# Kernel optimization log

Measured on AMD Instinct MI355X. Metric: run time of the kernel, lower is better.

## Reference

```python
import jax, jax.numpy as jnp
import numpy as np

BATCH, T, HID = 4, 2048, 1024
H = P = 1024  # input_dim and ssm_size (expand_ratio=1.0)
EPS = 1e-5
DISCRETIZATION = "IM"  # 'IM' or 'IMEX'


def setup_inputs() -> dict:
    key = jax.random.key(0)
    ks = jax.random.split(key, 10)
    std_b = 1.0 / np.sqrt(H)
    std_c = 1.0 / np.sqrt(P)
    u = lambda k, s, lo, hi: jax.random.uniform(k, s, jnp.float32, lo, hi)
    return {
        "hidden_states": jax.random.normal(ks[0], (BATCH, T, HID), jnp.float32),
        "Wi": jax.random.normal(ks[1], (H, HID), jnp.float32) / np.sqrt(HID),
        "Wg": jax.random.normal(ks[2], (H, HID), jnp.float32) / np.sqrt(HID),
        "Wo": jax.random.normal(ks[3], (HID, H), jnp.float32) / np.sqrt(H),
        "A_diag": u(ks[4], (P,), 0.0, 1.0),
        "B_param": u(ks[5], (P, H, 2), -std_b, std_b),
        "C_param": u(ks[6], (H, P, 2), -std_c, std_c),
        "D": jax.random.normal(ks[7], (H,), jnp.float32),
        "dt": u(ks[8], (P,), 0.0, 1.0),
        "norm_weight": jnp.ones((H,), jnp.float32),
    }


def _linoss(x, B_param, C_param, A_diag, dt_p, D):
    """LinOSS oscillatory SSM recurrence with complex B/C and diagonal A.
    x: (B,T,H) real input. State z,y in C^P (re/im stacked on last axis)."""
    A = jax.nn.relu(A_diag)       # (P,) nonneg frequencies
    dt = jax.nn.sigmoid(dt_p)     # (P,) timesteps in (0,1)
    # Bu_{re,im}[b,t,p] = sum_h x[b,t,h] * B_{re,im}[p,h]
    Bu = jnp.einsum('bth,phc->btpc', x, B_param)  # (B,T,P,2)
    if DISCRETIZATION == "IM":
        S = 1.0 / (1.0 + dt * dt * A)
        m11, m12, m21, m22 = S, -dt * A * S, dt * S, S
        f1, f2 = dt * S, dt * dt * S
    else:  # IMEX
        one = jnp.ones_like(dt)
        m11, m12, m21, m22 = one, -dt * A, dt, 1.0 - dt * dt * A
        f1, f2 = dt, dt * dt
    c = lambda v: v[None, :, None]  # broadcast (P,) -> (B,P,2)

    def step(carry, bu):
        z, y = carry  # each (B,P,2)
        z1 = c(m11) * z + c(m12) * y + c(f1) * bu
        y1 = c(m21) * z + c(m22) * y + c(f2) * bu
        return (z1, y1), y1

    z0 = jnp.zeros((x.shape[0], A.shape[0], 2), x.dtype)
    _, ys = jax.lax.scan(step, (z0, z0), jnp.swapaxes(Bu, 0, 1))
    ys = jnp.swapaxes(ys, 0, 1)  # (B,T,P,2)
    # o = Re(C @ y) + D * x
    o = (jnp.einsum('btp,hp->bth', ys[..., 0], C_param[..., 0])
         - jnp.einsum('btp,hp->bth', ys[..., 1], C_param[..., 1]))
    return o + x * D


def reference(hidden_states, Wi, Wg, Wo, A_diag, B_param, C_param, D, dt, norm_weight):
    x = hidden_states @ Wi.T                        # i_proj
    o = _linoss(x, B_param, C_param, A_diag, dt, D)  # fused_recurrent_linoss
    g = hidden_states @ Wg.T                        # g_proj
    # FusedRMSNormGated: rmsnorm(o) * weight * swish(g)
    o = o * jax.lax.rsqrt(jnp.mean(o * o, axis=-1, keepdims=True) + EPS) * norm_weight
    o = o * (g * jax.nn.sigmoid(g))
    return o @ Wo.T                                  # o_proj
```

## Files before the change

### kernel.cpp

```cpp
#include <hip/hip_runtime.h>
#include <hip/hip_bf16.h>
#include <math.h>

#define BB 4
#define TT 2048
#define HH 1024
#define PP 1024
#define MT 8192
#define C2 2048
#define NC 64
#define LCH 32

typedef __attribute__((ext_vector_type(8))) short  bf16x8;
typedef __attribute__((ext_vector_type(4))) float  f32x4;

__device__ __forceinline__ ushort f2bf(float f) {
    union { float f; unsigned u; } v; v.f = f;
    unsigned r = v.u + 0x7fffu + ((v.u >> 16) & 1u);
    return (ushort)(r >> 16);
}
__device__ __forceinline__ float bf2f(ushort h) {
    union { unsigned u; float f; } v; v.u = ((unsigned)h) << 16;
    return v.f;
}

__device__ __forceinline__ void gload16(const ushort* g, ushort* l) {
    __builtin_amdgcn_global_load_lds((const __attribute__((address_space(1))) void*)g,
                                     (__attribute__((address_space(3))) void*)l,
                                     16, 0, 0);
}
__device__ __forceinline__ void barrier_raw() { __builtin_amdgcn_s_barrier(); }
__device__ __forceinline__ void lgk0() { asm volatile("s_waitcnt lgkmcnt(0)" ::: "memory"); }
__device__ __forceinline__ void lgk8() { asm volatile("s_waitcnt lgkmcnt(8)" ::: "memory"); }
__device__ __forceinline__ void vm4()  { asm volatile("s_waitcnt vmcnt(4)"   ::: "memory"); }
__device__ __forceinline__ void vm6()  { asm volatile("s_waitcnt vmcnt(6)"   ::: "memory"); }
__device__ __forceinline__ void vm0()  { asm volatile("s_waitcnt vmcnt(0)"   ::: "memory"); }

#define HS4   (MT * HH / 4)
#define W4    (HH * HH / 4)
#define PREP_CONV  (HS4 + 3 * W4)
#define PREP_B     (PREP_CONV + PP * HH)
#define PREP_TOT   (PREP_B + HH * PP)

__global__ void prep_all(const float* __restrict__ hs, const float* __restrict__ Wi,
                         const float* __restrict__ Wg, const float* __restrict__ Wo,
                         const float* __restrict__ B_param, const float* __restrict__ C_param,
                         ushort* __restrict__ hsb, ushort* __restrict__ Wigb,
                         ushort* __restrict__ Wob, ushort* __restrict__ Bpkb,
                         ushort* __restrict__ Cpkb) {
    int i = blockIdx.x * 256 + threadIdx.x;
    if (i < PREP_CONV) {
        const float4* s;
        ushort4* d;
        if (i < HS4)              { s = (const float4*)hs + i;  d = (ushort4*)hsb + i; }
        else if (i < HS4 + 2*W4)  { int j = i - HS4;
                                    s = (const float4*)(j < W4 ? Wi : Wg) + (j < W4 ? j : j - W4);
                                    d = (ushort4*)Wigb + j; }
        else                      { int j = i - HS4 - 2*W4;
                                    s = (const float4*)Wo + j; d = (ushort4*)Wob + j; }
        float4 v = *s;
        ushort4 o;
        o.x = f2bf(v.x); o.y = f2bf(v.y); o.z = f2bf(v.z); o.w = f2bf(v.w);
        *d = o;
    } else if (i < PREP_B) {
        int idx = i - PREP_CONV;
        int p = idx >> 10;
        int h = idx & 1023;
        float2 v = ((const float2*)B_param)[idx];
        Bpkb[(size_t)p * HH + h]        = f2bf(v.x);
        Bpkb[(size_t)(p + PP) * HH + h] = f2bf(v.y);
    } else {
        int idx = i - PREP_B;
        int h = idx >> 10;
        int p = idx & 1023;
        float2 v = ((const float2*)C_param)[idx];
        Cpkb[(size_t)h * C2 + p]      = f2bf(v.x);
        Cpkb[(size_t)h * C2 + PP + p] = f2bf(-v.y);
    }
}

template<int BM, int STORE_BF16>
__global__ __launch_bounds__(512, 2) void gemm8p(
    const ushort* __restrict__ A, int lda,
    const ushort* __restrict__ B, int ldb,
    void* __restrict__ Cp, int ldc, int K, int nbx)
{
    constexpr int BN  = 256;
    constexpr int MR  = BM / 32;
    constexpr int MRH = MR / 2;
    constexpr int TA  = BM * 128;
    constexpr int TB  = BN * 128;
    __shared__ __align__(16) char smem[2 * TA + 2 * TB];

    const int bid = blockIdx.x;
    const int cpx = gridDim.x >> 3;
    const int wg  = (bid & 7) * cpx + (bid >> 3);
    const int by  = wg / nbx;
    const int bx  = wg - by * nbx;
    const int bm  = by * BM;
    const int bn  = bx * BN;

    const int tid  = threadIdx.x;
    const int wave = tid >> 6;
    const int lane = tid & 63;
    const int wr   = wave >> 2;
    const int wc   = wave & 3;
    const int lr   = lane & 15;
    const int kg   = lane >> 4;

    const int e  = (wave << 10) + ((lane << 4) ^ (((lane >> 3) & 7) << 4));
    const int r0 = e >> 7;
    const int c0 = (e & 127) >> 1;

    auto stA = [&](int bi, int u, int kt) {
        gload16(A + (size_t)(bm + u * 64 + r0) * lda + kt * 64 + c0,
                (ushort*)(smem + bi * TA + u * 8192 + (wave << 10)));
    };
    auto stB = [&](int bi, int u, int kt) {
        gload16(B + (size_t)(bn + u * 64 + r0) * ldb + kt * 64 + c0,
                (ushort*)(smem + 2 * TA + bi * TB + u * 8192 + (wave << 10)));
    };

    bf16x8 Af[MRH][2], Bf[4][2];
    auto ldsA = [&](int bi, int qm) {
#pragma unroll
        for (int f = 0; f < MRH; ++f)
#pragma unroll
            for (int kk = 0; kk < 2; ++kk) {
                int row = wr * (BM / 2) + qm * (BM / 4) + f * 16 + lr;
                int o = row * 128 + kk * 64 + kg * 16;
                o ^= (row & 7) << 4;
                Af[f][kk] = *(const bf16x8*)(smem + bi * TA + o);
            }
    };
    auto ldsBh = [&](int bi, int h) {
#pragma unroll
        for (int n = 0; n < 2; ++n)
#pragma unroll
            for (int kk = 0; kk < 2; ++kk) {
                int row = wc * 64 + (h * 2 + n) * 16 + lr;
                int o = row * 128 + kk * 64 + kg * 16;
                o ^= (row & 7) << 4;
                Bf[h * 2 + n][kk] = *(const bf16x8*)(smem + 2 * TA + bi * TB + o);
            }
    };

    f32x4 acc[MR][4];
#pragma unroll
    for (int m = 0; m < MR; ++m)
#pragma unroll
        for (int n = 0; n < 4; ++n)
#pragma unroll
            for (int i = 0; i < 4; ++i) acc[m][n][i] = 0.f;

    auto mfma16 = [&](int qm, int qn) {
        __builtin_amdgcn_s_setprio(1);
#pragma unroll
        for (int f = 0; f < MRH; ++f)
#pragma unroll
            for (int n2 = 0; n2 < 2; ++n2)
#pragma unroll
                for (int kk = 0; kk < 2; ++kk)
                    acc[qm * MRH + f][qn * 2 + n2] =
                        __builtin_amdgcn_mfma_f32_16x16x32_bf16(
                            Af[f][kk], Bf[qn * 2 + n2][kk],
                            acc[qm * MRH + f][qn * 2 + n2], 0, 0, 0);
        __builtin_amdgcn_s_setprio(0);
    };

    stA(0, 0, 0); stA(0, 1, 0); stA(0, 2, 0); stA(0, 3, 0);
    stB(0, 0, 0); stB(0, 1, 0); stB(0, 2, 0); stB(0, 3, 0);
    stB(1, 0, 1); stB(1, 1, 1); stB(1, 2, 1); stB(1, 3, 1);
    stA(1, 0, 1); stA(1, 2, 1);
    vm6();
    barrier_raw();

    const int nIter = K >> 7;
    for (int J = 0; J < nIter; ++J) {
        const bool pf  = (J + 1 < nIter);
        const int  kt1 = 2 * J + 1, kt2 = 2 * J + 2, kt3 = 2 * J + 3;
        ldsA(0, 0); ldsBh(0, 0);
        stA(1, 1, kt1); stA(1, 3, kt1);
        lgk8();
        barrier_raw(); lgk0(); mfma16(0, 0); barrier_raw();
        ldsBh(0, 1);
        barrier_raw(); lgk0(); mfma16(0, 1); barrier_raw();
        ldsA(0, 1);
        if (pf) { stB(0, 0, kt2); stB(0, 1, kt2); stB(0, 2, kt2); stB(0, 3, kt2); }
        barrier_raw(); lgk0(); mfma16(1, 0); barrier_raw();
        if (pf) { stA(0, 0, kt2); stA(0, 2, kt2); }
        barrier_raw(); lgk0(); mfma16(1, 1);
        if (pf) vm6(); else vm0();
        barrier_raw();
        ldsA(1, 0); ldsBh(1, 0);
        if (pf) { stA(0, 1, kt2); stA(0, 3, kt2); }
        lgk8();
        barrier_raw(); lgk0(); mfma16(0, 0); barrier_raw();
        ldsBh(1, 1);
        barrier_raw(); lgk0(); mfma16(0, 1); barrier_raw();
        ldsA(1, 1);
        if (pf) { stB(1, 0, kt3); stB(1, 1, kt3); stB(1, 2, kt3); stB(1, 3, kt3); }
        barrier_raw(); lgk0(); mfma16(1, 0); barrier_raw();
        if (pf) { stA(1, 0, kt3); stA(1, 2, kt3); }
        barrier_raw(); lgk0(); mfma16(1, 1);
        if (pf) vm6(); else vm0();
        barrier_raw();
    }

#pragma unroll
    for (int mf = 0; mf < MR; ++mf) {
#pragma unroll
        for (int n = 0; n < 4; ++n) {
            int col = bn + wc * 64 + n * 16 + lr;
#pragma unroll
            for (int i = 0; i < 4; ++i) {
                int row = bm + wr * (BM / 2) + mf * 16 + kg * 4 + i;
                float v = acc[mf][n][i];
                if (STORE_BF16)
                    ((ushort*)Cp)[(size_t)row * ldc + col] = f2bf(v);
                else
                    ((float*)Cp)[(size_t)row * ldc + col]  = v;
            }
        }
    }
}

template<int STORE_BF16>
__global__ __launch_bounds__(512, 2) void gemm4p(
    const ushort* __restrict__ A, int lda,
    const ushort* __restrict__ B, int ldb,
    void* __restrict__ Cp, int ldc, int K, int nbx)
{
    constexpr int BM = 128, BN = 256;
    constexpr int TA = BM * 128;
    constexpr int TB = BN * 128;
    __shared__ __align__(16) char smem[2 * TA + 2 * TB];

    const int bid = blockIdx.x;
    const int cpx = gridDim.x >> 3;
    const int wg  = (bid & 7) * cpx + (bid >> 3);
    const int by  = wg / nbx;
    const int bx  = wg - by * nbx;
    const int bm  = by * BM;
    const int bn  = bx * BN;

    const int tid  = threadIdx.x;
    const int wave = tid >> 6;
    const int lane = tid & 63;
    const int wr   = wave >> 2;
    const int wc   = wave & 3;
    const int lr   = lane & 15;
    const int kg   = lane >> 4;

    const int e  = (wave << 10) + ((lane << 4) ^ (((lane >> 3) & 7) << 4));
    const int r0 = e >> 7;
    const int c0 = (e & 127) >> 1;

    auto stA = [&](int bi, int u, int kt) {
        gload16(A + (size_t)(bm + u * 64 + r0) * lda + kt * 64 + c0,
                (ushort*)(smem + bi * TA + u * 8192 + (wave << 10)));
    };
    auto stB = [&](int bi, int u, int kt) {
        gload16(B + (size_t)(bn + u * 64 + r0) * ldb + kt * 64 + c0,
                (ushort*)(smem + 2 * TA + bi * TB + u * 8192 + (wave << 10)));
    };

    bf16x8 Af[2][2], Bf[4][2];
    auto ldsA = [&](int bi, int qm) {
#pragma unroll
        for (int f = 0; f < 2; ++f)
#pragma unroll
            for (int kk = 0; kk < 2; ++kk) {
                int row = wr * 64 + qm * 32 + f * 16 + lr;
                int o = row * 128 + kk * 64 + kg * 16;
                o ^= (row & 7) << 4;
                Af[f][kk] = *(const bf16x8*)(smem + bi * TA + o);
            }
    };
    auto ldsB = [&](int bi) {
#pragma unroll
        for (int n = 0; n < 4; ++n)
#pragma unroll
            for (int kk = 0; kk < 2; ++kk) {
                int row = wc * 64 + n * 16 + lr;
                int o = row * 128 + kk * 64 + kg * 16;
                o ^= (row & 7) << 4;
                Bf[n][kk] = *(const bf16x8*)(smem + 2 * TA + bi * TB + o);
            }
    };

    f32x4 acc[4][4];
#pragma unroll
    for (int m = 0; m < 4; ++m)
#pragma unroll
        for (int n = 0; n < 4; ++n)
#pragma unroll
            for (int i = 0; i < 4; ++i) acc[m][n][i] = 0.f;

    auto cl = [&](int qm) {
        __builtin_amdgcn_s_setprio(1);
#pragma unroll
        for (int f = 0; f < 2; ++f)
#pragma unroll
            for (int n = 0; n < 4; ++n)
#pragma unroll
                for (int kk = 0; kk < 2; ++kk)
                    acc[qm * 2 + f][n] =
                        __builtin_amdgcn_mfma_f32_16x16x32_bf16(
                            Af[f][kk], Bf[n][kk], acc[qm * 2 + f][n], 0, 0, 0);
        __builtin_amdgcn_s_setprio(0);
    };

    stB(0, 0, 0); stB(0, 1, 0); stB(0, 2, 0); stB(0, 3, 0);
    stA(0, 0, 0); stA(0, 1, 0);
    stB(1, 0, 1); stB(1, 1, 1); stB(1, 2, 1); stB(1, 3, 1);
    vm4();
    barrier_raw();

    const int nIter = K >> 7;
    for (int J = 0; J < nIter; ++J) {
        const bool pf  = (J + 1 < nIter);
        const int  kt1 = 2 * J + 1, kt2 = 2 * J + 2, kt3 = 2 * J + 3;
        ldsA(0, 0); ldsB(0);
        stA(1, 0, kt1); stA(1, 1, kt1);
        lgk8();
        barrier_raw();
        cl(0);
        lgk0();
        barrier_raw();
        ldsA(0, 1);
        if (pf) { stB(0, 0, kt2); stB(0, 1, kt2); stB(0, 2, kt2); stB(0, 3, kt2); }
        barrier_raw();
        cl(1);
        lgk0();
        if (pf) vm4(); else vm0();
        barrier_raw();
        ldsA(1, 0); ldsB(1);
        if (pf) { stA(0, 0, kt2); stA(0, 1, kt2); }
        lgk8();
        barrier_raw();
        cl(0);
        lgk0();
        barrier_raw();
        ldsA(1, 1);
        if (pf) { stB(1, 0, kt3); stB(1, 1, kt3); stB(1, 2, kt3); stB(1, 3, kt3); }
        barrier_raw();
        cl(1);
        lgk0();
        if (pf) vm4();
        barrier_raw();
    }

#pragma unroll
    for (int mf = 0; mf < 4; ++mf) {
#pragma unroll
        for (int n = 0; n < 4; ++n) {
            int col = bn + wc * 64 + n * 16 + lr;
#pragma unroll
            for (int i = 0; i < 4; ++i) {
                int row = bm + wr * 64 + mf * 16 + kg * 4 + i;
                float v = acc[mf][n][i];
                if (STORE_BF16)
                    ((ushort*)Cp)[(size_t)row * ldc + col] = f2bf(v);
                else
                    ((float*)Cp)[(size_t)row * ldc + col]  = v;
            }
        }
    }
}

__device__ __forceinline__ void linoss_coeffs(const float* A_diag, const float* dt_p,
                                              int p, float& m11, float& m12,
                                              float& m21, float& m22,
                                              float& f1, float& f2) {
    float A  = fmaxf(A_diag[p], 0.f);
    float dt = 1.f / (1.f + expf(-dt_p[p]));
    float S  = 1.f / (1.f + dt * dt * A);
    m11 = S;        m12 = -dt * A * S;
    m21 = dt * S;   m22 = S;
    f1  = dt * S;   f2  = dt * dt * S;
}

__global__ void scan_passA(const ushort* __restrict__ Bu,
                           const float* __restrict__ A_diag,
                           const float* __restrict__ dt_p,
                           float2* __restrict__ sEnd) {
    int c = blockIdx.x * 256 + threadIdx.x;
    int b = blockIdx.y;
    int j = blockIdx.z;
    float m11, m12, m21, m22, f1, f2;
    linoss_coeffs(A_diag, dt_p, c & 1023, m11, m12, m21, m22, f1, f2);
    const ushort* bu = Bu + ((size_t)(b * TT + j * LCH)) * C2 + c;
    float z = 0.f, y = 0.f;
#pragma unroll 8
    for (int i = 0; i < LCH; ++i) {
        float u  = bf2f(bu[(size_t)i * C2]);
        float z1 = m11 * z + m12 * y + f1 * u;
        float y1 = m21 * z + m22 * y + f2 * u;
        z = z1; y = y1;
    }
    sEnd[((size_t)j * BB + b) * C2 + c] = make_float2(z, y);
}

__global__ void scan_combine(const float* __restrict__ A_diag,
                             const float* __restrict__ dt_p,
                             const float2* __restrict__ sEnd,
                             float2* __restrict__ sInit) {
    int idx = blockIdx.x * 256 + threadIdx.x;
    int c = idx & (C2 - 1);
    int b = idx >> 11;
    float m11, m12, m21, m22, f1, f2;
    linoss_coeffs(A_diag, dt_p, c & 1023, m11, m12, m21, m22, f1, f2);
    float e11 = m11, e12 = m12, e21 = m21, e22 = m22;
#pragma unroll
    for (int s = 0; s < 5; ++s) {
        float n11 = e11 * e11 + e12 * e21;
        float n12 = e11 * e12 + e12 * e22;
        float n21 = e21 * e11 + e22 * e21;
        float n22 = e21 * e12 + e22 * e22;
        e11 = n11; e12 = n12; e21 = n21; e22 = n22;
    }
    float z = 0.f, y = 0.f;
    for (int j = 0; j < NC; ++j) {
        size_t off = ((size_t)j * BB + b) * C2 + c;
        sInit[off] = make_float2(z, y);
        float2 le = sEnd[off];
        float z1 = e11 * z + e12 * y + le.x;
        float y1 = e21 * z + e22 * y + le.y;
        z = z1; y = y1;
    }
}

__global__ void scan_passB(const ushort* __restrict__ Bu,
                           const float* __restrict__ A_diag,
                           const float* __restrict__ dt_p,
                           const float2* __restrict__ sInit,
                           ushort* __restrict__ YSb) {
    int c = blockIdx.x * 256 + threadIdx.x;
    int b = blockIdx.y;
    int j = blockIdx.z;
    float m11, m12, m21, m22, f1, f2;
    linoss_coeffs(A_diag, dt_p, c & 1023, m11, m12, m21, m22, f1, f2);
    float2 s0 = sInit[((size_t)j * BB + b) * C2 + c];
    float z = s0.x, y = s0.y;
    const ushort* bu = Bu  + ((size_t)(b * TT + j * LCH)) * C2 + c;
    ushort*       ys = YSb + ((size_t)(b * TT + j * LCH)) * C2 + c;
#pragma unroll 8
    for (int i = 0; i < LCH; ++i) {
        float u  = bf2f(bu[(size_t)i * C2]);
        float z1 = m11 * z + m12 * y + f1 * u;
        float y1 = m21 * z + m22 * y + f2 * u;
        z = z1; y = y1;
        ys[(size_t)i * C2] = f2bf(y);
    }
}

__global__ void rmsgate_kernel(const ushort* __restrict__ O,
                               const ushort* __restrict__ XGb,
                               const float* __restrict__ Dv,
                               const float* __restrict__ nw,
                               ushort* __restrict__ V) {
    int m = blockIdx.x;
    int t = threadIdx.x;
    ushort4 o4 = ((const ushort4*)(O + (size_t)m * HH))[t];
    ushort4 x4 = ((const ushort4*)(XGb + (size_t)m * C2))[t];
    float4  d4 = ((const float4*)Dv)[t];
    float of[4];
    of[0] = bf2f(o4.x) + d4.x * bf2f(x4.x);
    of[1] = bf2f(o4.y) + d4.y * bf2f(x4.y);
    of[2] = bf2f(o4.z) + d4.z * bf2f(x4.z);
    of[3] = bf2f(o4.w) + d4.w * bf2f(x4.w);
    float ss = of[0]*of[0] + of[1]*of[1] + of[2]*of[2] + of[3]*of[3];
#pragma unroll
    for (int o = 32; o > 0; o >>= 1) ss += __shfl_down(ss, o);
    __shared__ float wsum[4];
    if ((t & 63) == 0) wsum[t >> 6] = ss;
    __syncthreads();
    float tot = wsum[0] + wsum[1] + wsum[2] + wsum[3];
    float r = rsqrtf(tot * (1.f / (float)HH) + 1e-5f);

    ushort4 g4 = ((const ushort4*)(XGb + (size_t)m * C2 + HH))[t];
    float4  w4 = ((const float4*)nw)[t];
    float g[4] = {bf2f(g4.x), bf2f(g4.y), bf2f(g4.z), bf2f(g4.w)};
    float w[4] = {w4.x, w4.y, w4.z, w4.w};
    ushort4 vout;
    ushort* vo = &vout.x;
#pragma unroll
    for (int i = 0; i < 4; ++i) {
        float sw = g[i] / (1.f + expf(-g[i]));
        vo[i] = f2bf(of[i] * r * w[i] * sw);
    }
    ((ushort4*)(V + (size_t)m * HH))[t] = vout;
}

extern "C" void kernel_launch(void* const* d_in, const int* in_sizes, int n_in,
                              void* d_out, int out_size, void* d_ws, size_t ws_size,
                              hipStream_t stream) {
    const float* hs      = (const float*)d_in[0];
    const float* Wi      = (const float*)d_in[1];
    const float* Wg      = (const float*)d_in[2];
    const float* Wo      = (const float*)d_in[3];
    const float* A_diag  = (const float*)d_in[4];
    const float* B_param = (const float*)d_in[5];
    const float* C_param = (const float*)d_in[6];
    const float* Dv      = (const float*)d_in[7];
    const float* dtp     = (const float*)d_in[8];
    const float* nw      = (const float*)d_in[9];
    float* out = (float*)d_out;

    char* ws = (char*)d_ws;
    ushort* hsb  = (ushort*)ws;                                   ws += (size_t)MT * HH * 2;
    ushort* Wigb = (ushort*)ws;                                   ws += (size_t)C2 * HH * 2;
    ushort* Wob  = (ushort*)ws;                                   ws += (size_t)HH * HH * 2;
    ushort* Bpkb = (ushort*)ws;                                   ws += (size_t)C2 * HH * 2;
    ushort* Cpkb = (ushort*)ws;                                   ws += (size_t)HH * C2 * 2;
    ushort* XGb  = (ushort*)ws;                                   ws += (size_t)MT * C2 * 2;
    ushort* Bu   = (ushort*)ws;                                   ws += (size_t)MT * C2 * 2;
    ushort* YSb  = (ushort*)ws;                                   ws += (size_t)MT * C2 * 2;
    ushort* O    = (ushort*)ws;                                   ws += (size_t)MT * HH * 2;
    ushort* Vb   = (ushort*)ws;                                   ws += (size_t)MT * HH * 2;
    float2* sEnd  = (float2*)ws;                                  ws += (size_t)NC * BB * C2 * 8;
    float2* sInit = (float2*)ws;

    dim3 blk(256);

    prep_all<<<dim3(PREP_TOT / 256), blk, 0, stream>>>(
        hs, Wi, Wg, Wo, B_param, C_param, hsb, Wigb, Wob, Bpkb, Cpkb);

    gemm8p<256, 1><<<dim3(256), dim3(512), 0, stream>>>(
        hsb, HH, Wigb, HH, XGb, C2, HH, 8);

    gemm8p<256, 1><<<dim3(256), dim3(512), 0, stream>>>(
        XGb, C2, Bpkb, HH, Bu, C2, HH, 8);

    scan_passA<<<dim3(C2 / 256, BB, NC), blk, 0, stream>>>(Bu, A_diag, dtp, sEnd);
    scan_combine<<<dim3((BB * C2) / 256), blk, 0, stream>>>(A_diag, dtp, sEnd, sInit);
    scan_passB<<<dim3(C2 / 256, BB, NC), blk, 0, stream>>>(Bu, A_diag, dtp, sInit, YSb);

    gemm4p<1><<<dim3(256), dim3(512), 0, stream>>>(
        YSb, C2, Cpkb, C2, O, HH, C2, 4);

    rmsgate_kernel<<<dim3(MT), blk, 0, stream>>>(O, XGb, Dv, nw, Vb);

    gemm4p<0><<<dim3(256), dim3(512), 0, stream>>>(
        Vb, HH, Wob, HH, out, HH, HH, 4);
}
```

Baseline: 188.1 us.

## Use 128x128 tiles with 4-wave blocks and simpler double buffering for N=1024 GEMMs

New measurement: 187.9 us. Within noise of the previous version (-0.1%).

```diff
diff --git a/kernel.cpp b/kernel.cpp
--- a/kernel.cpp
+++ b/kernel.cpp
@@ -32,7 +32,6 @@
 __device__ __forceinline__ void barrier_raw() { __builtin_amdgcn_s_barrier(); }
 __device__ __forceinline__ void lgk0() { asm volatile("s_waitcnt lgkmcnt(0)" ::: "memory"); }
 __device__ __forceinline__ void lgk8() { asm volatile("s_waitcnt lgkmcnt(8)" ::: "memory"); }
-__device__ __forceinline__ void vm4()  { asm volatile("s_waitcnt vmcnt(4)"   ::: "memory"); }
 __device__ __forceinline__ void vm6()  { asm volatile("s_waitcnt vmcnt(6)"   ::: "memory"); }
 __device__ __forceinline__ void vm0()  { asm volatile("s_waitcnt vmcnt(0)"   ::: "memory"); }
 
@@ -226,12 +225,12 @@
 }
 
 template<int STORE_BF16>
-__global__ __launch_bounds__(512, 2) void gemm4p(
+__global__ __launch_bounds__(256, 2) void gemm2b(
     const ushort* __restrict__ A, int lda,
     const ushort* __restrict__ B, int ldb,
     void* __restrict__ Cp, int ldc, int K, int nbx)
 {
-    constexpr int BM = 128, BN = 256;
+    constexpr int BM = 128, BN = 128;
     constexpr int TA = BM * 128;
     constexpr int TB = BN * 128;
     __shared__ __align__(16) char smem[2 * TA + 2 * TB];
@@ -247,8 +246,8 @@
     const int tid  = threadIdx.x;
     const int wave = tid >> 6;
     const int lane = tid & 63;
-    const int wr   = wave >> 2;
-    const int wc   = wave & 3;
+    const int wr   = wave >> 1;
+    const int wc   = wave & 1;
     const int lr   = lane & 15;
     const int kg   = lane >> 4;
 
@@ -257,12 +256,12 @@
     const int c0 = (e & 127) >> 1;
 
     auto stA = [&](int bi, int u, int kt) {
-        gload16(A + (size_t)(bm + u * 64 + r0) * lda + kt * 64 + c0,
-                (ushort*)(smem + bi * TA + u * 8192 + (wave << 10)));
+        gload16(A + (size_t)(bm + u * 32 + r0) * lda + kt * 64 + c0,
+                (ushort*)(smem + bi * TA + u * 4096 + (wave << 10)));
     };
     auto stB = [&](int bi, int u, int kt) {
-        gload16(B + (size_t)(bn + u * 64 + r0) * ldb + kt * 64 + c0,
-                (ushort*)(smem + 2 * TA + bi * TB + u * 8192 + (wave << 10)));
+        gload16(B + (size_t)(bn + u * 32 + r0) * ldb + kt * 64 + c0,
+                (ushort*)(smem + 2 * TA + bi * TB + u * 4096 + (wave << 10)));
     };
 
     bf16x8 Af[2][2], Bf[4][2];
@@ -311,43 +310,29 @@
         __builtin_amdgcn_s_setprio(0);
     };
 
+    stA(0, 0, 0); stA(0, 1, 0); stA(0, 2, 0); stA(0, 3, 0);
     stB(0, 0, 0); stB(0, 1, 0); stB(0, 2, 0); stB(0, 3, 0);
-    stA(0, 0, 0); stA(0, 1, 0);
-    stB(1, 0, 1); stB(1, 1, 1); stB(1, 2, 1); stB(1, 3, 1);
-    vm4();
+    vm0();
     barrier_raw();
 
-    const int nIter = K >> 7;
-    for (int J = 0; J < nIter; ++J) {
-        const bool pf  = (J + 1 < nIter);
-        const int  kt1 = 2 * J + 1, kt2 = 2 * J + 2, kt3 = 2 * J + 3;
-        ldsA(0, 0); ldsB(0);
-        stA(1, 0, kt1); stA(1, 1, kt1);
-        lgk8();
+    const int nT = K >> 6;
+    for (int t = 0; t < nT; ++t) {
+        const int  bt = t & 1, b1 = bt ^ 1;
+        const bool pf = (t + 1 < nT);
+        ldsA(bt, 0); ldsB(bt);
+        if (pf) { stB(b1, 0, t + 1); stB(b1, 1, t + 1);
+                  stB(b1, 2, t + 1); stB(b1, 3, t + 1); }
         barrier_raw();
         cl(0);
         lgk0();
         barrier_raw();
-        ldsA(0, 1);
-        if (pf) { stB(0, 0, kt2); stB(0, 1, kt2); stB(0, 2, kt2); stB(0, 3, kt2); }
+        ldsA(bt, 1);
+        if (pf) { stA(b1, 0, t + 1); stA(b1, 1, t + 1);
+                  stA(b1, 2, t + 1); stA(b1, 3, t + 1); }
         barrier_raw();
         cl(1);
         lgk0();
-        if (pf) vm4(); else vm0();
-        barrier_raw();
-        ldsA(1, 0); ldsB(1);
-        if (pf) { stA(0, 0, kt2); stA(0, 1, kt2); }
-        lgk8();
-        barrier_raw();
-        cl(0);
-        lgk0();
-        barrier_raw();
-        ldsA(1, 1);
-        if (pf) { stB(1, 0, kt3); stB(1, 1, kt3); stB(1, 2, kt3); stB(1, 3, kt3); }
-        barrier_raw();
-        cl(1);
-        lgk0();
-        if (pf) vm4();
+        if (pf) vm0();
         barrier_raw();
     }
 
@@ -537,11 +522,11 @@
     scan_combine<<<dim3((BB * C2) / 256), blk, 0, stream>>>(A_diag, dtp, sEnd, sInit);
     scan_passB<<<dim3(C2 / 256, BB, NC), blk, 0, stream>>>(Bu, A_diag, dtp, sInit, YSb);
 
-    gemm4p<1><<<dim3(256), dim3(512), 0, stream>>>(
-        YSb, C2, Cpkb, C2, O, HH, C2, 4);
+    gemm2b<1><<<dim3(512), dim3(256), 0, stream>>>(
+        YSb, C2, Cpkb, C2, O, HH, C2, 8);
 
     rmsgate_kernel<<<dim3(MT), blk, 0, stream>>>(O, XGb, Dv, nw, Vb);
 
-    gemm4p<0><<<dim3(256), dim3(512), 0, stream>>>(
-        Vb, HH, Wob, HH, out, HH, HH, 4);
-}
+    gemm2b<0><<<dim3(512), dim3(256), 0, stream>>>(
+        Vb, HH, Wob, HH, out, HH, HH, 8);
+}
```
